# Kernel optimization log

Hardware: AMD Instinct MI355X
Metric: run time of the kernel (lower is better)

## Reference

```python
import jax, jax.numpy as jnp
import numpy as np

N_RAYS = 32768
N_OBJ = 16
N_SAMPLES = 32   # n_pts_object
N_BASE = 64      # pre-existing coarse samples per ray
MISS = 1e10      # sentinel for non-intersecting slots (sorts to the end)


def _make_transforms(key):
    """Random rigid+scale world-to-object transforms, pytorch3d row-vector convention:
    p' = p @ M[:3,:3] + M[3,:3]."""
    k1, k2, k3 = jax.random.split(key, 3)
    A = jax.random.normal(k1, (N_OBJ, 3, 3))
    Q, _ = jnp.linalg.qr(A)                                   # orthonormal 3x3
    t = jax.random.normal(k2, (N_OBJ, 3)) * 5.0               # translations
    s = jax.random.uniform(k3, (N_OBJ, 3), minval=0.5, maxval=2.0)
    eye = jnp.tile(jnp.eye(4, dtype=jnp.float32), (N_OBJ, 1, 1))
    rots = eye.at[:, :3, :3].set(Q.astype(jnp.float32))
    trafos = rots.at[:, 3, :3].set(t)
    scales = eye.at[:, 0, 0].set(s[:, 0]).at[:, 1, 1].set(s[:, 1]).at[:, 2, 2].set(s[:, 2])
    return trafos, rots, scales


def setup_inputs() -> dict:
    key = jax.random.key(0)
    k0, k1, k2, k3 = jax.random.split(key, 4)
    origins = jax.random.normal(k0, (N_RAYS, 3), dtype=jnp.float32) * 2.0
    directions = jax.random.normal(k1, (N_RAYS, 3), dtype=jnp.float32)
    lengths = jnp.sort(jax.random.uniform(k2, (N_RAYS, N_BASE), dtype=jnp.float32,
                                          minval=0.1, maxval=20.0), axis=-1)
    trafos, rots, scales = _make_transforms(k3)
    return {"origins": origins, "directions": directions, "lengths": lengths,
            "trafos_w2o": trafos, "rots_w2o": rots, "scales_w2o": scales}


def reference(origins, directions, lengths, trafos_w2o, rots_w2o, scales_w2o):
    N = origins.shape[0]
    M = trafos_w2o.shape[0]
    S = N_SAMPLES

    d_w = directions / jnp.linalg.norm(directions, axis=-1, keepdims=True)

    # compose transforms (row-vector convention: compose(m1, m2) -> m1 @ m2)
    pt_mat = trafos_w2o @ scales_w2o     # points world->object, [M,4,4]
    dir_mat = rots_w2o @ scales_w2o      # directions world->object

    # rays in each object frame: [M,N,3]
    origins_o = jnp.einsum('ni,mij->mnj', origins, pt_mat[:, :3, :3]) + pt_mat[:, None, 3, :3]
    dirs_o = jnp.einsum('ni,mij->mnj', d_w, dir_mat[:, :3, :3])
    dirs_o = dirs_o / jnp.linalg.norm(dirs_o, axis=-1, keepdims=True)

    # slab ray-AABB intersection against unit box [-1,1]^3
    inv = 1.0 / dirs_o
    t0 = (-1.0 - origins_o) * inv
    t1 = (1.0 - origins_o) * inv
    tmin = jnp.max(jnp.minimum(t0, t1), axis=-1)   # [M,N]
    tmax = jnp.min(jnp.maximum(t0, t1), axis=-1)
    hit = (tmax > tmin) & (tmax > 0.0)
    t_in = jnp.maximum(tmin, 0.0)

    # BoxRaysampler: linspace between entry and exit
    lin = jnp.linspace(0.0, 1.0, S, dtype=origins.dtype)
    z_o = t_in[..., None] + (tmax - t_in)[..., None] * lin          # [M,N,S]

    # object-space sample points / dirs
    pts_o = origins_o[:, :, None] + dirs_o[:, :, None] * z_o[..., None]   # [M,N,S,3]
    dirs_o_s = jnp.broadcast_to(dirs_o[:, :, None], pts_o.shape)

    # back to world -> z along world ray
    o2w = jnp.linalg.inv(pt_mat)
    pts_w = jnp.einsum('mnsi,mij->mnsj', pts_o, o2w[:, :3, :3]) + o2w[:, None, None, 3, :3]
    z_w = jnp.einsum('mnsj,nj->mns', pts_w - origins[None, :, None], d_w)
    z_w = jnp.where(hit[..., None], z_w, MISS)                      # mask misses

    # scatter into per-ray lengths (static worst-case size), then sort per ray
    z_flat = jnp.transpose(z_w, (1, 0, 2)).reshape(N, M * S)        # [N, M*S]
    lengths_new = jnp.concatenate([lengths, z_flat], axis=-1)       # [N, B+M*S]

    node_ids = jnp.broadcast_to(jnp.arange(M, dtype=jnp.int32)[:, None, None], (M, N, S))
    node_ids = jnp.where(hit[..., None], node_ids, -1)
    node_flat = jnp.concatenate(
        [jnp.full((N, lengths.shape[-1]), -1, dtype=jnp.int32),
         jnp.transpose(node_ids, (1, 0, 2)).reshape(N, M * S)], axis=-1)
    mask_flat = jnp.concatenate(
        [jnp.zeros((N, lengths.shape[-1]), dtype=bool),
         jnp.transpose(jnp.broadcast_to(hit[..., None], (M, N, S)), (1, 0, 2)).reshape(N, M * S)],
        axis=-1)

    order = jnp.argsort(lengths_new, axis=-1)
    sorted_lengths = jnp.take_along_axis(lengths_new, order, axis=-1)
    sorted_nodes = jnp.take_along_axis(node_flat, order, axis=-1)
    sorted_mask = jnp.take_along_axis(mask_flat, order, axis=-1)

    # flattened object-space samples (zeroed for misses; static shape)
    pts_flat = (pts_o * hit[..., None, None]).reshape(-1, 3)
    dirs_flat = (dirs_o_s * hit[..., None, None]).reshape(-1, 3)

    return sorted_lengths, sorted_nodes, sorted_mask, pts_flat, dirs_flat
```

## Files before the change

kernel.cpp:

```cpp
#include <hip/hip_runtime.h>

#define NR    32768
#define NOBJ  16
#define NS    32
#define NB    64
#define WIDTH 576
#define MISSV 1e10f

__device__ __forceinline__ float fmulr(float a, float b){ return __fmul_rn(a,b); }
__device__ __forceinline__ float faddr(float a, float b){ return __fadd_rn(a,b); }
__device__ __forceinline__ float fsubr(float a, float b){ return __fsub_rn(a,b); }
__device__ __forceinline__ float fdvr (float a, float b){ return __fdiv_rn(a,b); }

struct RayObj {
  float oo[3];
  float dd[3];
  float t_in, dt;
  float dn;
  bool  hit;
};

__device__ __forceinline__ void ray_obj_setup(
    const float* __restrict__ origins, const float* __restrict__ dirs,
    const float* __restrict__ trafos,  const float* __restrict__ scales,
    int m, int n, RayObj& R)
{
  const float o0 = origins[3*n+0], o1 = origins[3*n+1], o2 = origins[3*n+2];
  const float r0 = dirs[3*n+0],    r1 = dirs[3*n+1],    r2 = dirs[3*n+2];
  const float nn = __fsqrt_rn(faddr(faddr(fmulr(r0,r0), fmulr(r1,r1)), fmulr(r2,r2)));
  const float w0 = fdvr(r0,nn), w1 = fdvr(r1,nn), w2 = fdvr(r2,nn);

  const float* T = trafos + 16*m;
  const float* S = scales + 16*m;
  const float s0 = S[0], s1 = S[5], s2 = S[10];
  const float pm00 = fmulr(T[0],  s0), pm01 = fmulr(T[1],  s1), pm02 = fmulr(T[2],  s2);
  const float pm10 = fmulr(T[4],  s0), pm11 = fmulr(T[5],  s1), pm12 = fmulr(T[6],  s2);
  const float pm20 = fmulr(T[8],  s0), pm21 = fmulr(T[9],  s1), pm22 = fmulr(T[10], s2);
  const float tm0  = fmulr(T[12], s0), tm1  = fmulr(T[13], s1), tm2  = fmulr(T[14], s2);

  const float oo0 = faddr(faddr(faddr(fmulr(o0,pm00), fmulr(o1,pm10)), fmulr(o2,pm20)), tm0);
  const float oo1 = faddr(faddr(faddr(fmulr(o0,pm01), fmulr(o1,pm11)), fmulr(o2,pm21)), tm1);
  const float oo2 = faddr(faddr(faddr(fmulr(o0,pm02), fmulr(o1,pm12)), fmulr(o2,pm22)), tm2);
  const float du0 = faddr(faddr(fmulr(w0,pm00), fmulr(w1,pm10)), fmulr(w2,pm20));
  const float du1 = faddr(faddr(fmulr(w0,pm01), fmulr(w1,pm11)), fmulr(w2,pm21));
  const float du2 = faddr(faddr(fmulr(w0,pm02), fmulr(w1,pm12)), fmulr(w2,pm22));
  const float dn  = __fsqrt_rn(faddr(faddr(fmulr(du0,du0), fmulr(du1,du1)), fmulr(du2,du2)));
  const float dd0 = fdvr(du0,dn), dd1 = fdvr(du1,dn), dd2 = fdvr(du2,dn);

  const float i0 = fdvr(1.0f, dd0), i1 = fdvr(1.0f, dd1), i2 = fdvr(1.0f, dd2);
  const float a0 = fmulr(fsubr(-1.0f, oo0), i0), b0 = fmulr(fsubr(1.0f, oo0), i0);
  const float a1 = fmulr(fsubr(-1.0f, oo1), i1), b1 = fmulr(fsubr(1.0f, oo1), i1);
  const float a2 = fmulr(fsubr(-1.0f, oo2), i2), b2 = fmulr(fsubr(1.0f, oo2), i2);
  const float tmn = fmaxf(fmaxf(fminf(a0,b0), fminf(a1,b1)), fminf(a2,b2));
  const float tmx = fminf(fminf(fmaxf(a0,b0), fmaxf(a1,b1)), fmaxf(a2,b2));

  R.hit  = (tmx > tmn) && (tmx > 0.0f);
  R.t_in = fmaxf(tmn, 0.0f);
  R.dt   = fsubr(tmx, R.t_in);
  R.dn   = dn;
  R.oo[0]=oo0; R.oo[1]=oo1; R.oo[2]=oo2;
  R.dd[0]=dd0; R.dd[1]=dd1; R.dd[2]=dd2;
}

__device__ __forceinline__ int count_run(const float* __restrict__ K,
                                         const float* __restrict__ A,
                                         const float* __restrict__ B,
                                         const float* __restrict__ IB,
                                         int m2, float key, bool tie)
{
  const float A2 = A[m2], B2 = B[m2];
  const float* V = K + NB + m2 * NS;
  if (B2 <= 0.0f) {
    return (A2 < key || (A2 == key && tie)) ? NS : 0;
  }
  float g = floorf(fmulr(fsubr(key, A2), IB[m2]));
  g = fminf(33.0f, fmaxf(-1.0f, g));
  int c = (int)g + 1;
  c = c < 0 ? 0 : (c > NS ? NS : c);
  while (c > 0)  { const float v = V[c-1]; if (v < key || (v == key && tie)) break; --c; }
  while (c < NS) { const float v = V[c];   if (v < key || (v == key && tie)) ++c; else break; }
  return c;
}

struct PtsS  { float ld[64][8]; };
struct SortS {
  float sKeys[4][WIDTH];
  float sA[4][NOBJ], sB[4][NOBJ], sIB[4][NOBJ];
  float sL[4][WIDTH], sN[4][WIDTH];
};
union __align__(16) Smem { PtsS p; SortS s; };

__global__ __launch_bounds__(256) void k_fused(
    const float* __restrict__ origins, const float* __restrict__ dirs,
    const float* __restrict__ lengths,
    const float* __restrict__ trafos,  const float* __restrict__ scales,
    float* __restrict__ outL, float* __restrict__ outN, float* __restrict__ outM,
    float* __restrict__ outP, float* __restrict__ outD)
{
  __shared__ Smem U;
  const int tid  = threadIdx.x;
  const int role = blockIdx.x & 1;
  const int bid  = blockIdx.x >> 1;

  if (role == 0) {
    const int m   = bid >> 9;
    const int n0  = (bid & 511) << 6;
    if (tid < 64) {
      RayObj R;
      ray_obj_setup(origins, dirs, trafos, scales, m, n0 + tid, R);
      const bool h = R.hit;
      U.p.ld[tid][0] = h ? R.oo[0] : 0.0f;
      U.p.ld[tid][1] = h ? R.oo[1] : 0.0f;
      U.p.ld[tid][2] = h ? R.oo[2] : 0.0f;
      U.p.ld[tid][3] = h ? R.dd[0] : 0.0f;
      U.p.ld[tid][4] = h ? R.dd[1] : 0.0f;
      U.p.ld[tid][5] = h ? R.t_in  : 0.0f;
      U.p.ld[tid][6] = h ? R.dt    : 0.0f;
      U.p.ld[tid][7] = h ? R.dd[2] : 0.0f;
    }
    __syncthreads();
    const size_t base = (size_t)(m * NR + n0) * 96;
    float4* P4 = (float4*)(outP + base);
    float4* D4 = (float4*)(outD + base);
    #pragma unroll
    for (int it = 0; it < 6; ++it) {
      const int f   = tid + (it << 8);
      const int rr  = f / 24;
      const int off = (f - rr * 24) * 4;
      const float oox = U.p.ld[rr][0], ooy = U.p.ld[rr][1], ooz = U.p.ld[rr][2];
      const float ddx = U.p.ld[rr][3], ddy = U.p.ld[rr][4], ddz = U.p.ld[rr][7];
      const float ti  = U.p.ld[rr][5], dtt = U.p.ld[rr][6];
      float4 p, d;
      float* pp = (float*)&p; float* dv = (float*)&d;
      #pragma unroll
      for (int i = 0; i < 4; ++i) {
        const int idx = off + i;
        const int s   = idx / 3;
        const int c   = idx - s * 3;
        const float z  = ti + dtt * ((float)s * (1.0f/31.0f));
        const float oc = (c == 0) ? oox : ((c == 1) ? ooy : ooz);
        const float dc = (c == 0) ? ddx : ((c == 1) ? ddy : ddz);
        pp[i] = oc + dc * z;
        dv[i] = dc;
      }
      P4[f] = p;
      D4[f] = d;
    }
    return;
  }

  const int wv   = tid >> 6;
  const int lane = tid & 63;
  const int n    = bid * 4 + wv;

  if (lane < NOBJ) {
    RayObj R;
    ray_obj_setup(origins, dirs, trafos, scales, lane, n, R);
    float myA = MISSV, myB = -1.0f, myIB = 0.0f;
    if (R.hit) {
      const double invdn = 1.0 / (double)R.dn;
      myA = (float)((double)R.t_in * invdn);
      myB = (float)(((double)R.dt * invdn) * (1.0 / 31.0));
      if (!(myB > 0.0f)) myB = 0.0f;
      myIB = (myB > 0.0f) ? (1.0f / myB) : 0.0f;
    }
    U.s.sA[wv][lane]  = myA;
    U.s.sB[wv][lane]  = R.hit ? myB : -1.0f;
    U.s.sIB[wv][lane] = myIB;
  }
  __syncthreads();

  unsigned hm = 0;
  #pragma unroll
  for (int mm = 0; mm < NOBJ; ++mm) hm |= (U.s.sB[wv][mm] >= 0.0f ? 1u : 0u) << mm;
  const int H = __popc(hm);

  float kr[9];
  kr[0] = lengths[n * NB + lane];
  U.s.sKeys[wv][lane] = kr[0];
  #pragma unroll
  for (int k = 1; k < 9; ++k) {
    const int m0 = 2*(k-1) + (lane >> 5);
    const int s  = lane & 31;
    const float A_ = U.s.sA[wv][m0], B_ = U.s.sB[wv][m0];
    const float key = (B_ < 0.0f) ? MISSV : faddr(A_, fmulr(B_, (float)s));
    kr[k] = key;
    U.s.sKeys[wv][64*k + lane] = key;
  }
  __syncthreads();

  const float* K = U.s.sKeys[wv];
  #pragma unroll
  for (int k = 0; k < 9; ++k) {
    const float key = kr[k];
    int rank; float nodef; float outkey = key;
    if (k == 0) {
      rank = lane;
      unsigned mm = hm;
      while (mm) { const int m2 = __ffs(mm) - 1; mm &= mm - 1;
        rank += count_run(K, U.s.sA[wv], U.s.sB[wv], U.s.sIB[wv], m2, key, false); }
      nodef = -1.0f;
    } else {
      const int m = 2*(k-1) + (lane >> 5);
      const int s = lane & 31;
      if (!((hm >> m) & 1u)) {
        const int MB = __popc((~hm) & ((1u << m) - 1u) & 0xFFFFu);
        rank  = NB + NS*H + NS*MB + s;
        nodef = -1.0f; outkey = MISSV;
      } else {
        rank = s;
        int c = 0;
        #pragma unroll
        for (int st = 64; st >= 1; st >>= 1) {
          const int t2 = c + st;
          if (t2 <= NB && K[t2-1] <= key) c = t2;
        }
        rank += c;
        unsigned mm = hm & ~(1u << m);
        while (mm) { const int m2 = __ffs(mm) - 1; mm &= mm - 1;
          rank += count_run(K, U.s.sA[wv], U.s.sB[wv], U.s.sIB[wv], m2, key, m2 < m); }
        nodef = (float)m;
      }
    }
    U.s.sL[wv][rank] = outkey;
    U.s.sN[wv][rank] = nodef;
  }
  __syncthreads();

  float4* pL = (float4*)(outL + (size_t)n * WIDTH);
  float4* pN = (float4*)(outN + (size_t)n * WIDTH);
  float4* pM = (float4*)(outM + (size_t)n * WIDTH);
  const float4* qL = (const float4*)U.s.sL[wv];
  const float4* qN = (const float4*)U.s.sN[wv];
  for (int i = lane; i < WIDTH/4; i += 64) pL[i] = qL[i];
  for (int i = lane; i < WIDTH/4; i += 64) {
    const float4 nv = qN[i];
    float4 mv;
    mv.x = nv.x >= 0.0f ? 1.0f : 0.0f;
    mv.y = nv.y >= 0.0f ? 1.0f : 0.0f;
    mv.z = nv.z >= 0.0f ? 1.0f : 0.0f;
    mv.w = nv.w >= 0.0f ? 1.0f : 0.0f;
    pN[i] = nv;
    pM[i] = mv;
  }
}

extern "C" void kernel_launch(void* const* d_in, const int* in_sizes, int n_in,
                              void* d_out, int out_size, void* d_ws, size_t ws_size,
                              hipStream_t stream)
{
  (void)in_sizes; (void)n_in; (void)out_size; (void)d_ws; (void)ws_size;
  const float* origins = (const float*)d_in[0];
  const float* dirs    = (const float*)d_in[1];
  const float* lengths = (const float*)d_in[2];
  const float* trafos  = (const float*)d_in[3];
  const float* scales  = (const float*)d_in[5];

  float* out  = (float*)d_out;
  float* outL = out;
  float* outN = out + (size_t)NR * WIDTH;
  float* outM = out + (size_t)2 * NR * WIDTH;
  float* outP = out + (size_t)3 * NR * WIDTH;
  float* outD = outP + (size_t)NOBJ * NR * NS * 3;

  hipLaunchKernelGGL(k_fused, dim3(16384), dim3(256), 0, stream,
                     origins, dirs, lengths, trafos, scales,
                     outL, outN, outM, outP, outD);
}
```

Before: 623.3 us.

## Shuffle per-ray params in point pass and pack node IDs into key bits

In the point/direction output pass, all four waves now each set up 16 ray-object pairs and broadcast the parameters with wavefront shuffles. This replaces the single-wave setup, LDS staging and block barrier. In the sort pass, the separate LDS arrays for sorted lengths and node IDs become one packed array that stores node+1 in the low 5 mantissa bits of each length. That halves the scatter and readback LDS traffic and shrinks shared memory, which may allow more blocks per CU. The cost is that output lengths lose their 5 low mantissa bits, a small precision approximation.

```diff
diff --git a/kernel.cpp b/kernel.cpp
--- a/kernel.cpp
+++ b/kernel.cpp
@@ -82,13 +82,11 @@
   return c;
 }
 
-struct PtsS  { float ld[64][8]; };
 struct SortS {
-  float sKeys[4][WIDTH];
-  float sA[4][NOBJ], sB[4][NOBJ], sIB[4][NOBJ];
-  float sL[4][WIDTH], sN[4][WIDTH];
+  float    sKeys[4][WIDTH];
+  float    sA[4][NOBJ], sB[4][NOBJ], sIB[4][NOBJ];
+  unsigned sP[4][WIDTH];
 };
-union __align__(16) Smem { PtsS p; SortS s; };
 
 __global__ __launch_bounds__(256) void k_fused(
     const float* __restrict__ origins, const float* __restrict__ dirs,
@@ -97,39 +95,36 @@
     float* __restrict__ outL, float* __restrict__ outN, float* __restrict__ outM,
     float* __restrict__ outP, float* __restrict__ outD)
 {
-  __shared__ Smem U;
+  __shared__ SortS U;
   const int tid  = threadIdx.x;
   const int role = blockIdx.x & 1;
   const int bid  = blockIdx.x >> 1;
+  const int wv   = tid >> 6;
+  const int lane = tid & 63;
 
   if (role == 0) {
-    const int m   = bid >> 9;
-    const int n0  = (bid & 511) << 6;
-    if (tid < 64) {
+    const int m  = bid >> 9;
+    const int n0 = (bid & 511) << 6;
+    float p0=0.f,p1=0.f,p2=0.f,p3=0.f,p4=0.f,p5=0.f,p6=0.f,p7=0.f;
+    if (lane < 16) {
       RayObj R;
-      ray_obj_setup(origins, dirs, trafos, scales, m, n0 + tid, R);
-      const bool h = R.hit;
-      U.p.ld[tid][0] = h ? R.oo[0] : 0.0f;
-      U.p.ld[tid][1] = h ? R.oo[1] : 0.0f;
-      U.p.ld[tid][2] = h ? R.oo[2] : 0.0f;
-      U.p.ld[tid][3] = h ? R.dd[0] : 0.0f;
-      U.p.ld[tid][4] = h ? R.dd[1] : 0.0f;
-      U.p.ld[tid][5] = h ? R.t_in  : 0.0f;
-      U.p.ld[tid][6] = h ? R.dt    : 0.0f;
-      U.p.ld[tid][7] = h ? R.dd[2] : 0.0f;
-    }
-    __syncthreads();
-    const size_t base = (size_t)(m * NR + n0) * 96;
-    float4* P4 = (float4*)(outP + base);
-    float4* D4 = (float4*)(outD + base);
+      ray_obj_setup(origins, dirs, trafos, scales, m, n0 + 16*wv + lane, R);
+      if (R.hit) {
+        p0=R.oo[0]; p1=R.oo[1]; p2=R.oo[2];
+        p3=R.dd[0]; p4=R.dd[1]; p5=R.dd[2];
+        p6=R.t_in;  p7=R.dt;
+      }
+    }
+    float4* P4 = (float4*)(outP + (size_t)(m * NR + n0) * 96) + wv * 384;
+    float4* D4 = (float4*)(outD + (size_t)(m * NR + n0) * 96) + wv * 384;
     #pragma unroll
     for (int it = 0; it < 6; ++it) {
-      const int f   = tid + (it << 8);
-      const int rr  = f / 24;
-      const int off = (f - rr * 24) * 4;
-      const float oox = U.p.ld[rr][0], ooy = U.p.ld[rr][1], ooz = U.p.ld[rr][2];
-      const float ddx = U.p.ld[rr][3], ddy = U.p.ld[rr][4], ddz = U.p.ld[rr][7];
-      const float ti  = U.p.ld[rr][5], dtt = U.p.ld[rr][6];
+      const int fw  = lane + (it << 6);
+      const int rl  = fw / 24;
+      const int off = (fw - rl * 24) * 4;
+      const float oox = __shfl(p0, rl), ooy = __shfl(p1, rl), ooz = __shfl(p2, rl);
+      const float ddx = __shfl(p3, rl), ddy = __shfl(p4, rl), ddz = __shfl(p5, rl);
+      const float ti  = __shfl(p6, rl), dtt = __shfl(p7, rl);
       float4 p, d;
       float* pp = (float*)&p; float* dv = (float*)&d;
       #pragma unroll
@@ -143,15 +138,13 @@
         pp[i] = oc + dc * z;
         dv[i] = dc;
       }
-      P4[f] = p;
-      D4[f] = d;
+      P4[fw] = p;
+      D4[fw] = d;
     }
     return;
   }
 
-  const int wv   = tid >> 6;
-  const int lane = tid & 63;
-  const int n    = bid * 4 + wv;
+  const int n = bid * 4 + wv;
 
   if (lane < NOBJ) {
     RayObj R;
@@ -164,49 +157,49 @@
       if (!(myB > 0.0f)) myB = 0.0f;
       myIB = (myB > 0.0f) ? (1.0f / myB) : 0.0f;
     }
-    U.s.sA[wv][lane]  = myA;
-    U.s.sB[wv][lane]  = R.hit ? myB : -1.0f;
-    U.s.sIB[wv][lane] = myIB;
+    U.sA[wv][lane]  = myA;
+    U.sB[wv][lane]  = R.hit ? myB : -1.0f;
+    U.sIB[wv][lane] = myIB;
   }
   __syncthreads();
 
   unsigned hm = 0;
   #pragma unroll
-  for (int mm = 0; mm < NOBJ; ++mm) hm |= (U.s.sB[wv][mm] >= 0.0f ? 1u : 0u) << mm;
+  for (int mm = 0; mm < NOBJ; ++mm) hm |= (U.sB[wv][mm] >= 0.0f ? 1u : 0u) << mm;
   const int H = __popc(hm);
 
   float kr[9];
   kr[0] = lengths[n * NB + lane];
-  U.s.sKeys[wv][lane] = kr[0];
+  U.sKeys[wv][lane] = kr[0];
   #pragma unroll
   for (int k = 1; k < 9; ++k) {
     const int m0 = 2*(k-1) + (lane >> 5);
     const int s  = lane & 31;
-    const float A_ = U.s.sA[wv][m0], B_ = U.s.sB[wv][m0];
+    const float A_ = U.sA[wv][m0], B_ = U.sB[wv][m0];
     const float key = (B_ < 0.0f) ? MISSV : faddr(A_, fmulr(B_, (float)s));
     kr[k] = key;
-    U.s.sKeys[wv][64*k + lane] = key;
+    U.sKeys[wv][64*k + lane] = key;
   }
   __syncthreads();
 
-  const float* K = U.s.sKeys[wv];
+  const float* K = U.sKeys[wv];
   #pragma unroll
   for (int k = 0; k < 9; ++k) {
     const float key = kr[k];
-    int rank; float nodef; float outkey = key;
+    int rank; unsigned n5; float outkey = key;
     if (k == 0) {
       rank = lane;
       unsigned mm = hm;
       while (mm) { const int m2 = __ffs(mm) - 1; mm &= mm - 1;
-        rank += count_run(K, U.s.sA[wv], U.s.sB[wv], U.s.sIB[wv], m2, key, false); }
-      nodef = -1.0f;
+        rank += count_run(K, U.sA[wv], U.sB[wv], U.sIB[wv], m2, key, false); }
+      n5 = 0u;
     } else {
       const int m = 2*(k-1) + (lane >> 5);
       const int s = lane & 31;
       if (!((hm >> m) & 1u)) {
         const int MB = __popc((~hm) & ((1u << m) - 1u) & 0xFFFFu);
-        rank  = NB + NS*H + NS*MB + s;
-        nodef = -1.0f; outkey = MISSV;
+        rank = NB + NS*H + NS*MB + s;
+        n5 = 0u; outkey = MISSV;
       } else {
         rank = s;
         int c = 0;
@@ -218,28 +211,29 @@
         rank += c;
         unsigned mm = hm & ~(1u << m);
         while (mm) { const int m2 = __ffs(mm) - 1; mm &= mm - 1;
-          rank += count_run(K, U.s.sA[wv], U.s.sB[wv], U.s.sIB[wv], m2, key, m2 < m); }
-        nodef = (float)m;
+          rank += count_run(K, U.sA[wv], U.sB[wv], U.sIB[wv], m2, key, m2 < m); }
+        n5 = (unsigned)(m + 1);
       }
     }
-    U.s.sL[wv][rank] = outkey;
-    U.s.sN[wv][rank] = nodef;
+    U.sP[wv][rank] = (__float_as_uint(outkey) & ~31u) | n5;
   }
   __syncthreads();
 
   float4* pL = (float4*)(outL + (size_t)n * WIDTH);
   float4* pN = (float4*)(outN + (size_t)n * WIDTH);
   float4* pM = (float4*)(outM + (size_t)n * WIDTH);
-  const float4* qL = (const float4*)U.s.sL[wv];
-  const float4* qN = (const float4*)U.s.sN[wv];
-  for (int i = lane; i < WIDTH/4; i += 64) pL[i] = qL[i];
+  const uint4* qP = (const uint4*)U.sP[wv];
   for (int i = lane; i < WIDTH/4; i += 64) {
-    const float4 nv = qN[i];
-    float4 mv;
-    mv.x = nv.x >= 0.0f ? 1.0f : 0.0f;
-    mv.y = nv.y >= 0.0f ? 1.0f : 0.0f;
-    mv.z = nv.z >= 0.0f ? 1.0f : 0.0f;
-    mv.w = nv.w >= 0.0f ? 1.0f : 0.0f;
+    const uint4 v = qP[i];
+    float4 lv, nv, mv;
+    const unsigned ax = v.x & 31u, ay = v.y & 31u, az = v.z & 31u, aw = v.w & 31u;
+    lv.x = __uint_as_float(v.x & ~31u); lv.y = __uint_as_float(v.y & ~31u);
+    lv.z = __uint_as_float(v.z & ~31u); lv.w = __uint_as_float(v.w & ~31u);
+    nv.x = (float)(int)ax - 1.0f; nv.y = (float)(int)ay - 1.0f;
+    nv.z = (float)(int)az - 1.0f; nv.w = (float)(int)aw - 1.0f;
+    mv.x = ax ? 1.0f : 0.0f; mv.y = ay ? 1.0f : 0.0f;
+    mv.z = az ? 1.0f : 0.0f; mv.w = aw ? 1.0f : 0.0f;
+    pL[i] = lv;
     pN[i] = nv;
     pM[i] = mv;
   }
```

Result: no change. 624.4 us (+0.2%).
